# Performance work log

Hardware: AMD Instinct MI355X
Metric: run time of the kernel (lower is better)

Reference implementation:

```python
import jax, jax.numpy as jnp
import numpy as np
from jax import lax

B, T, D, L = 64, 512, 1024, 32


def setup_inputs() -> dict:
    key = jax.random.key(0)
    k = jax.random.split(key, 8)
    x = jax.random.normal(k[0], (B, T, D), dtype=jnp.float32)
    mask = jnp.ones((B, T), dtype=bool)
    labels = jax.random.randint(k[1], (B, T), 0, L)
    W = jax.random.normal(k[2], (D, L), dtype=jnp.float32) / np.sqrt(D)
    b = jnp.zeros((L,), dtype=jnp.float32)
    transitions = jax.random.normal(k[3], (L, L), dtype=jnp.float32) * 0.1
    start_transitions = jax.random.normal(k[4], (L,), dtype=jnp.float32) * 0.1
    end_transitions = jax.random.normal(k[5], (L,), dtype=jnp.float32) * 0.1
    return {"x": x, "mask": mask, "labels": labels, "W": W, "b": b,
            "transitions": transitions, "start_transitions": start_transitions,
            "end_transitions": end_transitions}


def _log_partition(logits, mask, transitions, start_t, end_t):
    # logits: [B,T,L], mask: [B,T] bool. AllenNLP _input_likelihood.
    alpha0 = start_t[None, :] + logits[:, 0]  # [B,L]
    logits_t = jnp.swapaxes(logits, 0, 1)[1:]  # [T-1,B,L]
    mask_t = jnp.swapaxes(mask, 0, 1)[1:]      # [T-1,B]

    def step(alpha, inp):
        logit, m = inp  # [B,L], [B]
        # inner[b,i,j] = alpha[b,i] + transitions[i,j] + logit[b,j]
        inner = alpha[:, :, None] + transitions[None, :, :] + logit[:, None, :]
        new = jax.nn.logsumexp(inner, axis=1)
        return jnp.where(m[:, None], new, alpha), None

    alpha, _ = lax.scan(step, alpha0, (logits_t, mask_t))
    return jax.nn.logsumexp(alpha + end_t[None, :], axis=-1)  # [B]


def _joint_score(logits, tags, mask, transitions, start_t, end_t):
    # AllenNLP _joint_likelihood, vectorized over time.
    maskf = mask.astype(logits.dtype)
    score = start_t[tags[:, 0]]
    trans = transitions[tags[:, :-1], tags[:, 1:]]  # [B,T-1]
    score = score + jnp.sum(trans * maskf[:, 1:], axis=1)
    emit = jnp.take_along_axis(logits[:, :-1], tags[:, :-1, None], axis=2)[..., 0]
    score = score + jnp.sum(emit * maskf[:, :-1], axis=1)
    lengths = jnp.sum(mask.astype(jnp.int32), axis=1)
    last_tags = jnp.take_along_axis(tags, (lengths - 1)[:, None], axis=1)[:, 0]
    score = score + end_t[last_tags]
    last_emit = jnp.take_along_axis(logits[:, -1], last_tags[:, None], axis=1)[:, 0]
    score = score + last_emit * maskf[:, -1]
    return score  # [B]


def reference(x, mask, labels, W, b, transitions, start_transitions, end_transitions):
    logits = jnp.einsum('btd,dl->btl', x, W) + b  # Linear classifier
    probabilities = jax.nn.softmax(logits, axis=-1)
    logZ = _log_partition(logits, mask, transitions, start_transitions, end_transitions)
    gold = _joint_score(logits, labels, mask, transitions, start_transitions, end_transitions)
    log_likelihood = jnp.sum(gold - logZ)
    loss = -log_likelihood
    return probabilities, loss
```

## Files before the change

kernel.cpp:

```cpp
#include <hip/hip_runtime.h>

#define OUT_LOSS_IDX 1048576

typedef __attribute__((ext_vector_type(4)))  float f32x4;
typedef __attribute__((ext_vector_type(16))) float f32x16;
typedef __attribute__((ext_vector_type(4)))  int i32x4;
typedef __attribute__((ext_vector_type(4)))  unsigned u32x4;
typedef __attribute__((ext_vector_type(8)))  short bf16x8;

__device__ __forceinline__ unsigned short f32_to_bf16(float f) {
    unsigned u = __float_as_uint(f);
    unsigned r = (u + 0x7FFFu + ((u >> 16) & 1u)) >> 16;
    return (unsigned short)r;
}
__device__ __forceinline__ unsigned packbf(float lo, float hi) {
    return __builtin_amdgcn_perm(__float_as_uint(hi) + 0x8000u,
                                 __float_as_uint(lo) + 0x8000u, 0x07060302u);
}

__global__ void k0_wt(const float* __restrict__ W, unsigned short* __restrict__ Wt,
                      float* __restrict__ loss) {
    int idx = blockIdx.x * 256 + threadIdx.x;
    int k = idx >> 5, c = idx & 31;
    Wt[c * 1024 + k] = f32_to_bf16(W[idx]);
    if (idx == 0) loss[0] = 0.f;
}

__global__ __launch_bounds__(64) void k1_gemm(
    const float* __restrict__ x, const unsigned short* __restrict__ Wt,
    const float* __restrict__ bias, float* __restrict__ logits,
    float* __restrict__ probs) {
    const int lane = threadIdx.x;
    const int m = lane & 15, quad = lane >> 4;
    const int r0 = blockIdx.x * 16;

    const float* xa = x + (size_t)(r0 + m) * 1024 + quad * 8;
    const unsigned short* wb0 = Wt + (size_t)m * 1024 + quad * 8;
    const unsigned short* wb1 = Wt + (size_t)(m + 16) * 1024 + quad * 8;

    f32x4 acc0 = {0.f, 0.f, 0.f, 0.f};
    f32x4 acc1 = {0.f, 0.f, 0.f, 0.f};

    #pragma unroll 4
    for (int ks = 0; ks < 32; ++ks) {
        f32x4 a0 = *(const f32x4*)(xa + ks * 32);
        f32x4 a1 = *(const f32x4*)(xa + ks * 32 + 4);
        bf16x8 b0 = *(const bf16x8*)(wb0 + ks * 32);
        bf16x8 b1 = *(const bf16x8*)(wb1 + ks * 32);
        bf16x8 af;
        af[0] = (short)f32_to_bf16(a0[0]); af[1] = (short)f32_to_bf16(a0[1]);
        af[2] = (short)f32_to_bf16(a0[2]); af[3] = (short)f32_to_bf16(a0[3]);
        af[4] = (short)f32_to_bf16(a1[0]); af[5] = (short)f32_to_bf16(a1[1]);
        af[6] = (short)f32_to_bf16(a1[2]); af[7] = (short)f32_to_bf16(a1[3]);
        acc0 = __builtin_amdgcn_mfma_f32_16x16x32_bf16(af, b0, acc0, 0, 0, 0);
        acc1 = __builtin_amdgcn_mfma_f32_16x16x32_bf16(af, b1, acc1, 0, 0, 0);
    }
    const float bc0 = bias[m], bc1 = bias[16 + m];
    #pragma unroll
    for (int r = 0; r < 4; ++r) {
        int row = r0 + quad * 4 + r;
        float l0 = acc0[r] + bc0;
        float l1 = acc1[r] + bc1;
        logits[row * 32 + m] = l0;
        logits[row * 32 + 16 + m] = l1;
        float mx = fmaxf(l0, l1);
        #pragma unroll
        for (int d = 1; d < 16; d <<= 1) mx = fmaxf(mx, __shfl_xor(mx, d, 64));
        float e0 = __expf(l0 - mx), e1 = __expf(l1 - mx);
        float s = e0 + e1;
        #pragma unroll
        for (int d = 1; d < 16; d <<= 1) s += __shfl_xor(s, d, 64);
        float inv = 1.0f / s;
        probs[row * 32 + m] = e0 * inv;
        probs[row * 32 + 16 + m] = e1 * inv;
    }
}

__global__ __launch_bounds__(256, 1) void k3a_chunks(
    const float* __restrict__ logits, const int* __restrict__ mask,
    const float* __restrict__ trans, float* __restrict__ Gws,
    float* __restrict__ chunkLog) {
    __shared__ float sElt[128 * 32];
    __shared__ int smaskL[128];

    const int tid = threadIdx.x;
    const int b = blockIdx.x >> 2, a = blockIdx.x & 3;
    const int w = tid >> 6, lane = tid & 63;
    const int h = lane >> 5, col = lane & 31;

    const float* src = logits + (size_t)b * 16384 + (128 * a + 1) * 32;
    #pragma unroll
    for (int q = 0; q < 4; ++q) {
        int slot = q * 256 + tid;
        f32x4 v = *(const f32x4*)&src[slot * 4];
        f32x4 e = {__expf(v[0]), __expf(v[1]), __expf(v[2]), __expf(v[3])};
        *(f32x4*)&sElt[slot * 4] = e;
    }
    if (tid < 128) {
        int t = 128 * a + 1 + tid;
        smaskL[tid] = (t < 512) ? mask[b * 512 + t] : 0;
    }
    __syncthreads();

    bf16x8 a1, a2;
    #pragma unroll
    for (int j = 0; j < 8; ++j) {
        a1[j] = (short)f32_to_bf16(__expf(trans[(8 * h + j) * 32 + col]));
        a2[j] = (short)f32_to_bf16(__expf(trans[(16 + 8 * h + j) * 32 + col]));
    }

    float c[16];
    #pragma unroll
    for (int r = 0; r < 16; ++r)
        c[r] = (((r & 3) + 8 * (r >> 2) + 4 * h) == col) ? 1.f : 0.f;
    int esum = 0;

    for (int tl = 0; tl < 32; ++tl) {
        const int tt = 32 * w + tl;
        unsigned d0 = packbf(c[0],  c[1]),  d1 = packbf(c[2],  c[3]);
        unsigned d2 = packbf(c[4],  c[5]),  d3 = packbf(c[6],  c[7]);
        unsigned d4 = packbf(c[8],  c[9]),  d5 = packbf(c[10], c[11]);
        unsigned d6 = packbf(c[12], c[13]), d7 = packbf(c[14], c[15]);
        unsigned x0 = (unsigned)__shfl_xor((int)d0, 32, 64);
        unsigned x1 = (unsigned)__shfl_xor((int)d1, 32, 64);
        unsigned x2 = (unsigned)__shfl_xor((int)d2, 32, 64);
        unsigned x3 = (unsigned)__shfl_xor((int)d3, 32, 64);
        unsigned x4 = (unsigned)__shfl_xor((int)d4, 32, 64);
        unsigned x5 = (unsigned)__shfl_xor((int)d5, 32, 64);
        unsigned x6 = (unsigned)__shfl_xor((int)d6, 32, 64);
        unsigned x7 = (unsigned)__shfl_xor((int)d7, 32, 64);
        u32x4 b0w = {h ? x2 : d0, h ? x3 : d1, h ? d2 : x0, h ? d3 : x1};
        u32x4 b1w = {h ? x6 : d4, h ? x7 : d5, h ? d6 : x4, h ? d7 : x5};
        bf16x8 b0 = __builtin_bit_cast(bf16x8, b0w);
        bf16x8 b1 = __builtin_bit_cast(bf16x8, b1w);

        f32x16 zz = {};
        f32x16 acc = __builtin_amdgcn_mfma_f32_32x32x16_bf16(a1, b0, zz, 0, 0, 0);
        acc = __builtin_amdgcn_mfma_f32_32x32x16_bf16(a2, b1, acc, 0, 0, 0);

        const f32x4* ep = (const f32x4*)&sElt[tt * 32];
        f32x4 e0 = ep[h], e1 = ep[2 + h], e2 = ep[4 + h], e3 = ep[6 + h];
        const int mk = smaskL[tt];

        int sb = __builtin_amdgcn_readfirstlane(__float_as_int(c[0]));
        int ee = ((sb >> 23) & 0xff) - 127;
        ee = ee < -60 ? -60 : (ee > 60 ? 60 : ee);
        float sc = __int_as_float((127 - ee) << 23);
        esum += ee;

        #pragma unroll
        for (int r = 0; r < 16; ++r) {
            float ev = (r < 4 ? e0[r & 3] : r < 8 ? e1[r & 3] : r < 12 ? e2[r & 3] : e3[r & 3]);
            float qn = acc[r] * (ev * sc);
            float qa = c[r] * sc;
            c[r] = mk ? qn : qa;
        }
    }

    const int cc = 4 * a + w;
    float* gw = Gws + (((size_t)(b * 16 + cc)) << 10);
    #pragma unroll
    for (int r = 0; r < 16; ++r)
        gw[((r & 3) + 8 * (r >> 2) + 4 * h) * 32 + col] = c[r];
    if (lane == 0)
        chunkLog[b * 16 + cc] = (float)esum * 0.6931471805599453f;
}

__global__ __launch_bounds__(64, 1) void k3b_combine(
    const float* __restrict__ logits, const int* __restrict__ mask,
    const int* __restrict__ labels, const float* __restrict__ trans,
    const float* __restrict__ start_t, const float* __restrict__ end_t,
    const float* __restrict__ Gws, const float* __restrict__ chunkLog,
    float* __restrict__ loss_out) {
    __shared__ __align__(16) float pbuf[2][32];
    __shared__ int smaskL[512];

    const int b = blockIdx.x, lane = threadIdx.x;
    const int j = lane & 31;
    const int base = b * 512;

    #pragma unroll
    for (int it = 0; it < 2; ++it) {
        int idx = it * 64 + lane;
        *(i32x4*)&smaskL[idx * 4] = *(const i32x4*)&mask[base + idx * 4];
    }
    float p = __expf(start_t[j] + logits[(size_t)b * 16384 + j]);
    float logC = 0.f;
    pbuf[0][j] = p;
    __syncthreads();

    for (int cc = 0; cc < 16; ++cc) {
        const float* g = Gws + ((((size_t)(b * 16 + cc)) << 10) + j * 32);
        f32x4 g0 = *(const f32x4*)&g[0],  g1 = *(const f32x4*)&g[4];
        f32x4 g2 = *(const f32x4*)&g[8],  g3 = *(const f32x4*)&g[12];
        f32x4 g4 = *(const f32x4*)&g[16], g5 = *(const f32x4*)&g[20];
        f32x4 g6 = *(const f32x4*)&g[24], g7 = *(const f32x4*)&g[28];
        const float* pb = pbuf[cc & 1];
        f32x4 p0 = *(const f32x4*)&pb[0],  p1 = *(const f32x4*)&pb[4];
        f32x4 p2 = *(const f32x4*)&pb[8],  p3 = *(const f32x4*)&pb[12];
        f32x4 p4 = *(const f32x4*)&pb[16], p5 = *(const f32x4*)&pb[20];
        f32x4 p6 = *(const f32x4*)&pb[24], p7 = *(const f32x4*)&pb[28];
        float r0 = p0[0];
        float s0 = 0.f, s1 = 0.f, s2 = 0.f, s3 = 0.f;
        s0 = fmaf(p0[0], g0[0], s0); s1 = fmaf(p0[1], g0[1], s1);
        s2 = fmaf(p0[2], g0[2], s2); s3 = fmaf(p0[3], g0[3], s3);
        s0 = fmaf(p1[0], g1[0], s0); s1 = fmaf(p1[1], g1[1], s1);
        s2 = fmaf(p1[2], g1[2], s2); s3 = fmaf(p1[3], g1[3], s3);
        s0 = fmaf(p2[0], g2[0], s0); s1 = fmaf(p2[1], g2[1], s1);
        s2 = fmaf(p2[2], g2[2], s2); s3 = fmaf(p2[3], g2[3], s3);
        s0 = fmaf(p3[0], g3[0], s0); s1 = fmaf(p3[1], g3[1], s1);
        s2 = fmaf(p3[2], g3[2], s2); s3 = fmaf(p3[3], g3[3], s3);
        s0 = fmaf(p4[0], g4[0], s0); s1 = fmaf(p4[1], g4[1], s1);
        s2 = fmaf(p4[2], g4[2], s2); s3 = fmaf(p4[3], g4[3], s3);
        s0 = fmaf(p5[0], g5[0], s0); s1 = fmaf(p5[1], g5[1], s1);
        s2 = fmaf(p5[2], g5[2], s2); s3 = fmaf(p5[3], g5[3], s3);
        s0 = fmaf(p6[0], g6[0], s0); s1 = fmaf(p6[1], g6[1], s1);
        s2 = fmaf(p6[2], g6[2], s2); s3 = fmaf(p6[3], g6[3], s3);
        s0 = fmaf(p7[0], g7[0], s0); s1 = fmaf(p7[1], g7[1], s1);
        s2 = fmaf(p7[2], g7[2], s2); s3 = fmaf(p7[3], g7[3], s3);
        float s = (s0 + s1) + (s2 + s3);
        p = s * __builtin_amdgcn_rcpf(r0);
        pbuf[(cc + 1) & 1][j] = p;
        logC += __logf(r0);
    }
    float clsum = 0.f;
    #pragma unroll
    for (int cc = 0; cc < 16; ++cc) clsum += chunkLog[b * 16 + cc];

    float f = logC + clsum + __logf(p) + end_t[j];
    float mx = f;
    #pragma unroll
    for (int d = 1; d < 32; d <<= 1) mx = fmaxf(mx, __shfl_xor(mx, d, 64));
    float e = __expf(f - mx), se = e;
    #pragma unroll
    for (int d = 1; d < 32; d <<= 1) se += __shfl_xor(se, d, 64);
    float logZb = mx + __logf(se);

    const int t0 = lane * 8;
    const int* lb = labels + base + t0;
    i32x4 la = *(const i32x4*)&lb[0];
    i32x4 lc = *(const i32x4*)&lb[4];
    int tg[8] = {la[0], la[1], la[2], la[3], lc[0], lc[1], lc[2], lc[3]};
    int prev = (lane == 0) ? 0 : labels[base + t0 - 1];
    float part = 0.f;
    int cnt = 0;
    #pragma unroll
    for (int r = 0; r < 8; ++r) {
        int t = t0 + r;
        int mk = smaskL[t];
        float mf = mk ? 1.f : 0.f;
        cnt += mk ? 1 : 0;
        int tag = tg[r];
        if (t > 0) part += trans[prev * 32 + tag] * mf;
        if (t < 511) part += logits[(size_t)b * 16384 + t * 32 + tag] * mf;
        prev = tag;
    }
    #pragma unroll
    for (int d = 1; d < 64; d <<= 1) {
        part += __shfl_xor(part, d, 64);
        cnt += __shfl_xor(cnt, d, 64);
    }
    if (lane == 0) {
        int len = cnt;
        int first = labels[base];
        int last = labels[base + len - 1];
        float g = part + start_t[first] + end_t[last];
        g += logits[(size_t)b * 16384 + 511 * 32 + last] * (smaskL[511] ? 1.f : 0.f);
        atomicAdd(loss_out, logZb - g);
    }
}

extern "C" void kernel_launch(void* const* d_in, const int* in_sizes, int n_in,
                              void* d_out, int out_size, void* d_ws, size_t ws_size,
                              hipStream_t stream) {
    const float* x       = (const float*)d_in[0];
    const int* mk        = (const int*)d_in[1];
    const int* labels    = (const int*)d_in[2];
    const float* W       = (const float*)d_in[3];
    const float* bias    = (const float*)d_in[4];
    const float* trans   = (const float*)d_in[5];
    const float* start_t = (const float*)d_in[6];
    const float* end_t   = (const float*)d_in[7];

    float* probs = (float*)d_out;
    float* loss  = probs + OUT_LOSS_IDX;
    float* ws = (float*)d_ws;
    float* logits = ws;
    unsigned short* Wt = (unsigned short*)(ws + 1048576);
    float* Gws = ws + 1048576 + 16384;
    float* chunkLog = Gws + 1048576;

    k0_wt<<<128, 256, 0, stream>>>(W, Wt, loss);
    k1_gemm<<<2048, 64, 0, stream>>>(x, Wt, bias, logits, probs);
    k3a_chunks<<<256, 256, 0, stream>>>(logits, mk, trans, Gws, chunkLog);
    k3b_combine<<<64, 64, 0, stream>>>(logits, mk, labels, trans, start_t, end_t,
                                       Gws, chunkLog, loss);
}
```

Baseline: 239.4 us.

## Fuse logits GEMM with chunked CRF forward scan and prefetch combine matrices

Merges the GEMM/softmax kernel and the chunked forward-algorithm kernel into one kernel. Each 256-thread block computes the logits for its 128-timestep chunk and writes their exponentials straight into shared memory before running the per-wave MFMA scan. This drops a launch and the reload of logits from global memory. Chunk boundaries shift to start at 128*a, and the very first step is skipped. The combine kernel now prefetches the next chunk's transfer matrix while the current one is applied. The trade-off is that the GEMM, which streams all of x, now runs as 1024 waves at one block per CU instead of 2048 small blocks, which may expose less memory parallelism.

```diff
diff --git a/kernel.cpp b/kernel.cpp
--- a/kernel.cpp
+++ b/kernel.cpp
@@ -16,6 +16,45 @@
 __device__ __forceinline__ unsigned packbf(float lo, float hi) {
     return __builtin_amdgcn_perm(__float_as_uint(hi) + 0x8000u,
                                  __float_as_uint(lo) + 0x8000u, 0x07060302u);
+}
+__device__ __forceinline__ void make_bfrags(const float* c, int h, bf16x8& b0, bf16x8& b1) {
+    unsigned d0 = packbf(c[0],  c[1]),  d1 = packbf(c[2],  c[3]);
+    unsigned d2 = packbf(c[4],  c[5]),  d3 = packbf(c[6],  c[7]);
+    unsigned d4 = packbf(c[8],  c[9]),  d5 = packbf(c[10], c[11]);
+    unsigned d6 = packbf(c[12], c[13]), d7 = packbf(c[14], c[15]);
+    unsigned x0 = (unsigned)__shfl_xor((int)d0, 32, 64);
+    unsigned x1 = (unsigned)__shfl_xor((int)d1, 32, 64);
+    unsigned x2 = (unsigned)__shfl_xor((int)d2, 32, 64);
+    unsigned x3 = (unsigned)__shfl_xor((int)d3, 32, 64);
+    unsigned x4 = (unsigned)__shfl_xor((int)d4, 32, 64);
+    unsigned x5 = (unsigned)__shfl_xor((int)d5, 32, 64);
+    unsigned x6 = (unsigned)__shfl_xor((int)d6, 32, 64);
+    unsigned x7 = (unsigned)__shfl_xor((int)d7, 32, 64);
+    u32x4 b0w = {h ? x2 : d0, h ? x3 : d1, h ? d2 : x0, h ? d3 : x1};
+    u32x4 b1w = {h ? x6 : d4, h ? x7 : d5, h ? d6 : x4, h ? d7 : x5};
+    b0 = __builtin_bit_cast(bf16x8, b0w);
+    b1 = __builtin_bit_cast(bf16x8, b1w);
+}
+__device__ __forceinline__ void crf_step(float* c, const f32x4* ep, int h, int mk,
+                                         bf16x8 a1, bf16x8 a2, int& esum) {
+    bf16x8 b0, b1;
+    make_bfrags(c, h, b0, b1);
+    f32x16 zz = {};
+    f32x16 acc = __builtin_amdgcn_mfma_f32_32x32x16_bf16(a1, b0, zz, 0, 0, 0);
+    acc = __builtin_amdgcn_mfma_f32_32x32x16_bf16(a2, b1, acc, 0, 0, 0);
+    f32x4 e0 = ep[h], e1 = ep[2 + h], e2 = ep[4 + h], e3 = ep[6 + h];
+    int sb = __builtin_amdgcn_readfirstlane(__float_as_int(c[0]));
+    int ee = ((sb >> 23) & 0xff) - 127;
+    ee = ee < -60 ? -60 : (ee > 60 ? 60 : ee);
+    float sc = __int_as_float((127 - ee) << 23);
+    esum += ee;
+    #pragma unroll
+    for (int r = 0; r < 16; ++r) {
+        float ev = (r < 4 ? e0[r & 3] : r < 8 ? e1[r & 3] : r < 12 ? e2[r & 3] : e3[r & 3]);
+        float qn = acc[r] * (ev * sc);
+        float qa = c[r] * sc;
+        c[r] = mk ? qn : qa;
+    }
 }
 
 __global__ void k0_wt(const float* __restrict__ W, unsigned short* __restrict__ Wt,
@@ -26,59 +65,11 @@
     if (idx == 0) loss[0] = 0.f;
 }
 
-__global__ __launch_bounds__(64) void k1_gemm(
+__global__ __launch_bounds__(256, 1) void kA_gemm_chunks(
     const float* __restrict__ x, const unsigned short* __restrict__ Wt,
-    const float* __restrict__ bias, float* __restrict__ logits,
-    float* __restrict__ probs) {
-    const int lane = threadIdx.x;
-    const int m = lane & 15, quad = lane >> 4;
-    const int r0 = blockIdx.x * 16;
-
-    const float* xa = x + (size_t)(r0 + m) * 1024 + quad * 8;
-    const unsigned short* wb0 = Wt + (size_t)m * 1024 + quad * 8;
-    const unsigned short* wb1 = Wt + (size_t)(m + 16) * 1024 + quad * 8;
-
-    f32x4 acc0 = {0.f, 0.f, 0.f, 0.f};
-    f32x4 acc1 = {0.f, 0.f, 0.f, 0.f};
-
-    #pragma unroll 4
-    for (int ks = 0; ks < 32; ++ks) {
-        f32x4 a0 = *(const f32x4*)(xa + ks * 32);
-        f32x4 a1 = *(const f32x4*)(xa + ks * 32 + 4);
-        bf16x8 b0 = *(const bf16x8*)(wb0 + ks * 32);
-        bf16x8 b1 = *(const bf16x8*)(wb1 + ks * 32);
-        bf16x8 af;
-        af[0] = (short)f32_to_bf16(a0[0]); af[1] = (short)f32_to_bf16(a0[1]);
-        af[2] = (short)f32_to_bf16(a0[2]); af[3] = (short)f32_to_bf16(a0[3]);
-        af[4] = (short)f32_to_bf16(a1[0]); af[5] = (short)f32_to_bf16(a1[1]);
-        af[6] = (short)f32_to_bf16(a1[2]); af[7] = (short)f32_to_bf16(a1[3]);
-        acc0 = __builtin_amdgcn_mfma_f32_16x16x32_bf16(af, b0, acc0, 0, 0, 0);
-        acc1 = __builtin_amdgcn_mfma_f32_16x16x32_bf16(af, b1, acc1, 0, 0, 0);
-    }
-    const float bc0 = bias[m], bc1 = bias[16 + m];
-    #pragma unroll
-    for (int r = 0; r < 4; ++r) {
-        int row = r0 + quad * 4 + r;
-        float l0 = acc0[r] + bc0;
-        float l1 = acc1[r] + bc1;
-        logits[row * 32 + m] = l0;
-        logits[row * 32 + 16 + m] = l1;
-        float mx = fmaxf(l0, l1);
-        #pragma unroll
-        for (int d = 1; d < 16; d <<= 1) mx = fmaxf(mx, __shfl_xor(mx, d, 64));
-        float e0 = __expf(l0 - mx), e1 = __expf(l1 - mx);
-        float s = e0 + e1;
-        #pragma unroll
-        for (int d = 1; d < 16; d <<= 1) s += __shfl_xor(s, d, 64);
-        float inv = 1.0f / s;
-        probs[row * 32 + m] = e0 * inv;
-        probs[row * 32 + 16 + m] = e1 * inv;
-    }
-}
-
-__global__ __launch_bounds__(256, 1) void k3a_chunks(
-    const float* __restrict__ logits, const int* __restrict__ mask,
-    const float* __restrict__ trans, float* __restrict__ Gws,
+    const float* __restrict__ bias, const int* __restrict__ mask,
+    const float* __restrict__ trans, float* __restrict__ logits,
+    float* __restrict__ probs, float* __restrict__ Gws,
     float* __restrict__ chunkLog) {
     __shared__ float sElt[128 * 32];
     __shared__ int smaskL[128];
@@ -86,75 +77,86 @@
     const int tid = threadIdx.x;
     const int b = blockIdx.x >> 2, a = blockIdx.x & 3;
     const int w = tid >> 6, lane = tid & 63;
+    const int m = lane & 15, quad = lane >> 4;
     const int h = lane >> 5, col = lane & 31;
-
-    const float* src = logits + (size_t)b * 16384 + (128 * a + 1) * 32;
-    #pragma unroll
-    for (int q = 0; q < 4; ++q) {
-        int slot = q * 256 + tid;
-        f32x4 v = *(const f32x4*)&src[slot * 4];
-        f32x4 e = {__expf(v[0]), __expf(v[1]), __expf(v[2]), __expf(v[3])};
-        *(f32x4*)&sElt[slot * 4] = e;
-    }
-    if (tid < 128) {
-        int t = 128 * a + 1 + tid;
-        smaskL[tid] = (t < 512) ? mask[b * 512 + t] : 0;
-    }
-    __syncthreads();
-
-    bf16x8 a1, a2;
+    const int R0 = b * 512 + a * 128;
+    const int rw = R0 + 32 * w;
+
+    if (lane < 32) smaskL[w * 32 + lane] = mask[b * 512 + a * 128 + w * 32 + lane];
+
+    const float* xa0 = x + (size_t)(rw + m) * 1024 + quad * 8;
+    const float* xa1 = x + (size_t)(rw + 16 + m) * 1024 + quad * 8;
+    const unsigned short* wb0 = Wt + (size_t)m * 1024 + quad * 8;
+    const unsigned short* wb1 = Wt + (size_t)(m + 16) * 1024 + quad * 8;
+
+    f32x4 acc00 = {0.f, 0.f, 0.f, 0.f}, acc01 = {0.f, 0.f, 0.f, 0.f};
+    f32x4 acc10 = {0.f, 0.f, 0.f, 0.f}, acc11 = {0.f, 0.f, 0.f, 0.f};
+
+    #pragma unroll 2
+    for (int ks = 0; ks < 32; ++ks) {
+        f32x4 p0 = *(const f32x4*)(xa0 + ks * 32);
+        f32x4 p1 = *(const f32x4*)(xa0 + ks * 32 + 4);
+        f32x4 q0 = *(const f32x4*)(xa1 + ks * 32);
+        f32x4 q1 = *(const f32x4*)(xa1 + ks * 32 + 4);
+        bf16x8 b0 = *(const bf16x8*)(wb0 + ks * 32);
+        bf16x8 b1 = *(const bf16x8*)(wb1 + ks * 32);
+        bf16x8 af0, af1;
+        af0[0] = (short)f32_to_bf16(p0[0]); af0[1] = (short)f32_to_bf16(p0[1]);
+        af0[2] = (short)f32_to_bf16(p0[2]); af0[3] = (short)f32_to_bf16(p0[3]);
+        af0[4] = (short)f32_to_bf16(p1[0]); af0[5] = (short)f32_to_bf16(p1[1]);
+        af0[6] = (short)f32_to_bf16(p1[2]); af0[7] = (short)f32_to_bf16(p1[3]);
+        af1[0] = (short)f32_to_bf16(q0[0]); af1[1] = (short)f32_to_bf16(q0[1]);
+        af1[2] = (short)f32_to_bf16(q0[2]); af1[3] = (short)f32_to_bf16(q0[3]);
+        af1[4] = (short)f32_to_bf16(q1[0]); af1[5] = (short)f32_to_bf16(q1[1]);
+        af1[6] = (short)f32_to_bf16(q1[2]); af1[7] = (short)f32_to_bf16(q1[3]);
+        acc00 = __builtin_amdgcn_mfma_f32_16x16x32_bf16(af0, b0, acc00, 0, 0, 0);
+        acc01 = __builtin_amdgcn_mfma_f32_16x16x32_bf16(af0, b1, acc01, 0, 0, 0);
+        acc10 = __builtin_amdgcn_mfma_f32_16x16x32_bf16(af1, b0, acc10, 0, 0, 0);
+        acc11 = __builtin_amdgcn_mfma_f32_16x16x32_bf16(af1, b1, acc11, 0, 0, 0);
+    }
+
+    const float bc0 = bias[m], bc1 = bias[16 + m];
+    #pragma unroll
+    for (int tt = 0; tt < 2; ++tt) {
+        #pragma unroll
+        for (int r = 0; r < 4; ++r) {
+            float l0 = (tt ? acc10[r] : acc00[r]) + bc0;
+            float l1 = (tt ? acc11[r] : acc01[r]) + bc1;
+            int lrow = 32 * w + 16 * tt + quad * 4 + r;
+            int grow = R0 + lrow;
+            logits[grow * 32 + m] = l0;
+            logits[grow * 32 + 16 + m] = l1;
+            sElt[lrow * 32 + m] = __expf(l0);
+            sElt[lrow * 32 + 16 + m] = __expf(l1);
+            float mx = fmaxf(l0, l1);
+            #pragma unroll
+            for (int d = 1; d < 16; d <<= 1) mx = fmaxf(mx, __shfl_xor(mx, d, 64));
+            float e0 = __expf(l0 - mx), e1 = __expf(l1 - mx);
+            float s = e0 + e1;
+            #pragma unroll
+            for (int d = 1; d < 16; d <<= 1) s += __shfl_xor(s, d, 64);
+            float inv = 1.0f / s;
+            probs[grow * 32 + m] = e0 * inv;
+            probs[grow * 32 + 16 + m] = e1 * inv;
+        }
+    }
+
+    bf16x8 a1t, a2t;
     #pragma unroll
     for (int j = 0; j < 8; ++j) {
-        a1[j] = (short)f32_to_bf16(__expf(trans[(8 * h + j) * 32 + col]));
-        a2[j] = (short)f32_to_bf16(__expf(trans[(16 + 8 * h + j) * 32 + col]));
-    }
-
+        a1t[j] = (short)f32_to_bf16(__expf(trans[(8 * h + j) * 32 + col]));
+        a2t[j] = (short)f32_to_bf16(__expf(trans[(16 + 8 * h + j) * 32 + col]));
+    }
     float c[16];
     #pragma unroll
     for (int r = 0; r < 16; ++r)
         c[r] = (((r & 3) + 8 * (r >> 2) + 4 * h) == col) ? 1.f : 0.f;
     int esum = 0;
 
-    for (int tl = 0; tl < 32; ++tl) {
-        const int tt = 32 * w + tl;
-        unsigned d0 = packbf(c[0],  c[1]),  d1 = packbf(c[2],  c[3]);
-        unsigned d2 = packbf(c[4],  c[5]),  d3 = packbf(c[6],  c[7]);
-        unsigned d4 = packbf(c[8],  c[9]),  d5 = packbf(c[10], c[11]);
-        unsigned d6 = packbf(c[12], c[13]), d7 = packbf(c[14], c[15]);
-        unsigned x0 = (unsigned)__shfl_xor((int)d0, 32, 64);
-        unsigned x1 = (unsigned)__shfl_xor((int)d1, 32, 64);
-        unsigned x2 = (unsigned)__shfl_xor((int)d2, 32, 64);
-        unsigned x3 = (unsigned)__shfl_xor((int)d3, 32, 64);
-        unsigned x4 = (unsigned)__shfl_xor((int)d4, 32, 64);
-        unsigned x5 = (unsigned)__shfl_xor((int)d5, 32, 64);
-        unsigned x6 = (unsigned)__shfl_xor((int)d6, 32, 64);
-        unsigned x7 = (unsigned)__shfl_xor((int)d7, 32, 64);
-        u32x4 b0w = {h ? x2 : d0, h ? x3 : d1, h ? d2 : x0, h ? d3 : x1};
-        u32x4 b1w = {h ? x6 : d4, h ? x7 : d5, h ? d6 : x4, h ? d7 : x5};
-        bf16x8 b0 = __builtin_bit_cast(bf16x8, b0w);
-        bf16x8 b1 = __builtin_bit_cast(bf16x8, b1w);
-
-        f32x16 zz = {};
-        f32x16 acc = __builtin_amdgcn_mfma_f32_32x32x16_bf16(a1, b0, zz, 0, 0, 0);
-        acc = __builtin_amdgcn_mfma_f32_32x32x16_bf16(a2, b1, acc, 0, 0, 0);
-
-        const f32x4* ep = (const f32x4*)&sElt[tt * 32];
-        f32x4 e0 = ep[h], e1 = ep[2 + h], e2 = ep[4 + h], e3 = ep[6 + h];
-        const int mk = smaskL[tt];
-
-        int sb = __builtin_amdgcn_readfirstlane(__float_as_int(c[0]));
-        int ee = ((sb >> 23) & 0xff) - 127;
-        ee = ee < -60 ? -60 : (ee > 60 ? 60 : ee);
-        float sc = __int_as_float((127 - ee) << 23);
-        esum += ee;
-
-        #pragma unroll
-        for (int r = 0; r < 16; ++r) {
-            float ev = (r < 4 ? e0[r & 3] : r < 8 ? e1[r & 3] : r < 12 ? e2[r & 3] : e3[r & 3]);
-            float qn = acc[r] * (ev * sc);
-            float qa = c[r] * sc;
-            c[r] = mk ? qn : qa;
-        }
+    const int tl0 = (a == 0 && w == 0) ? 1 : 0;
+    for (int tl = tl0; tl < 32; ++tl) {
+        int lrow = 32 * w + tl;
+        crf_step(c, (const f32x4*)&sElt[lrow * 32], h, smaskL[lrow], a1t, a2t, esum);
     }
 
     const int cc = 4 * a + w;
@@ -166,7 +168,7 @@
         chunkLog[b * 16 + cc] = (float)esum * 0.6931471805599453f;
 }
 
-__global__ __launch_bounds__(64, 1) void k3b_combine(
+__global__ __launch_bounds__(64, 1) void kB_combine(
     const float* __restrict__ logits, const int* __restrict__ mask,
     const int* __restrict__ labels, const float* __restrict__ trans,
     const float* __restrict__ start_t, const float* __restrict__ end_t,
@@ -184,17 +186,26 @@
         int idx = it * 64 + lane;
         *(i32x4*)&smaskL[idx * 4] = *(const i32x4*)&mask[base + idx * 4];
     }
+    const float* gbase = Gws + (((size_t)(b * 16)) << 10) + j * 32;
+    f32x4 g0 = *(const f32x4*)&gbase[0],  g1 = *(const f32x4*)&gbase[4];
+    f32x4 g2 = *(const f32x4*)&gbase[8],  g3 = *(const f32x4*)&gbase[12];
+    f32x4 g4 = *(const f32x4*)&gbase[16], g5 = *(const f32x4*)&gbase[20];
+    f32x4 g6 = *(const f32x4*)&gbase[24], g7 = *(const f32x4*)&gbase[28];
+
     float p = __expf(start_t[j] + logits[(size_t)b * 16384 + j]);
     float logC = 0.f;
     pbuf[0][j] = p;
     __syncthreads();
 
     for (int cc = 0; cc < 16; ++cc) {
-        const float* g = Gws + ((((size_t)(b * 16 + cc)) << 10) + j * 32);
-        f32x4 g0 = *(const f32x4*)&g[0],  g1 = *(const f32x4*)&g[4];
-        f32x4 g2 = *(const f32x4*)&g[8],  g3 = *(const f32x4*)&g[12];
-        f32x4 g4 = *(const f32x4*)&g[16], g5 = *(const f32x4*)&g[20];
-        f32x4 g6 = *(const f32x4*)&g[24], g7 = *(const f32x4*)&g[28];
+        const float* gn = gbase + (((size_t)(cc + 1)) << 10);
+        f32x4 n0, n1, n2, n3, n4, n5, n6, n7;
+        if (cc < 15) {
+            n0 = *(const f32x4*)&gn[0];  n1 = *(const f32x4*)&gn[4];
+            n2 = *(const f32x4*)&gn[8];  n3 = *(const f32x4*)&gn[12];
+            n4 = *(const f32x4*)&gn[16]; n5 = *(const f32x4*)&gn[20];
+            n6 = *(const f32x4*)&gn[24]; n7 = *(const f32x4*)&gn[28];
+        }
         const float* pb = pbuf[cc & 1];
         f32x4 p0 = *(const f32x4*)&pb[0],  p1 = *(const f32x4*)&pb[4];
         f32x4 p2 = *(const f32x4*)&pb[8],  p3 = *(const f32x4*)&pb[12];
@@ -222,6 +233,7 @@
         p = s * __builtin_amdgcn_rcpf(r0);
         pbuf[(cc + 1) & 1][j] = p;
         logC += __logf(r0);
+        g0 = n0; g1 = n1; g2 = n2; g3 = n3; g4 = n4; g5 = n5; g6 = n6; g7 = n7;
     }
     float clsum = 0.f;
     #pragma unroll
@@ -291,8 +303,8 @@
     float* chunkLog = Gws + 1048576;
 
     k0_wt<<<128, 256, 0, stream>>>(W, Wt, loss);
-    k1_gemm<<<2048, 64, 0, stream>>>(x, Wt, bias, logits, probs);
-    k3a_chunks<<<256, 256, 0, stream>>>(logits, mk, trans, Gws, chunkLog);
-    k3b_combine<<<64, 64, 0, stream>>>(logits, mk, labels, trans, start_t, end_t,
-                                       Gws, chunkLog, loss);
-}
+    kA_gemm_chunks<<<256, 256, 0, stream>>>(x, Wt, bias, mk, trans,
+                                            logits, probs, Gws, chunkLog);
+    kB_combine<<<64, 64, 0, stream>>>(logits, mk, labels, trans, start_t, end_t,
+                                      Gws, chunkLog, loss);
+}
```

Result: no change. 244.1 us (+2.0%).
